# Kernel optimization log

Hardware: AMD Instinct MI355X
Metric: run time of the kernel (lower is better)

## Reference

```python
import jax, jax.numpy as jnp
import numpy as np

B, C, H, W = 4, 64, 64, 64
CQK = C // 8


def setup_inputs() -> dict:
    key = jax.random.key(0)
    ks = jax.random.split(key, 4)
    x = jax.random.normal(ks[0], (B, C, H, W), dtype=jnp.float32)
    Wq = jax.random.normal(ks[1], (CQK, C), dtype=jnp.float32) * (1.0 / np.sqrt(C))
    bq = jnp.zeros((CQK,), dtype=jnp.float32)
    Wk = jax.random.normal(ks[2], (CQK, C), dtype=jnp.float32) * (1.0 / np.sqrt(C))
    bk = jnp.zeros((CQK,), dtype=jnp.float32)
    Wv = jax.random.normal(ks[3], (C, C), dtype=jnp.float32) * (1.0 / np.sqrt(C))
    bv = jnp.zeros((C,), dtype=jnp.float32)
    gamma = jnp.ones((1,), dtype=jnp.float32)
    return {"x": x, "Wq": Wq, "bq": bq, "Wk": Wk, "bk": bk,
            "Wv": Wv, "bv": bv, "gamma": gamma}


def reference(x, Wq, bq, Wk, bk, Wv, bv, gamma):
    b, c, h, w = x.shape
    n = h * w
    xf = x.reshape(b, c, n)                      # [B, C, N]
    # 1x1 convs == per-pixel linear over channels
    q = jnp.einsum('oc,bcn->bon', Wq, xf) + bq[:, None]   # [B, C/8, N]
    k = jnp.einsum('oc,bcn->bon', Wk, xf) + bk[:, None]   # [B, C/8, N]
    v = jnp.einsum('oc,bcn->bon', Wv, xf) + bv[:, None]   # [B, C, N]
    # attention_map[b,i,j] = <q[:, i], k[:, j]>; softmax over j
    attn = jax.nn.softmax(jnp.einsum('bci,bcj->bij', q, k), axis=-1)  # [B, N, N]
    # out[b,c,i] = sum_j v[b,c,j] * attn[b,i,j]  (bmm(V, attn^T))
    out = jnp.einsum('bcj,bij->bci', v, attn).reshape(b, c, h, w)
    return gamma * out + x
```

## Files before the change

### kernel.cpp

```cpp
#include <hip/hip_runtime.h>
#include <hip/hip_bf16.h>
#include <math.h>

#define NPIX 4096

typedef __attribute__((ext_vector_type(8))) short s8;
typedef __attribute__((ext_vector_type(16))) float f16v;

static __device__ __forceinline__ unsigned packbf2(float a, float b) {
    union { __hip_bfloat162 h; unsigned u; } x;
    x.h = __float22bfloat162_rn(make_float2(a, b));
    return x.u;
}
static __device__ __forceinline__ float2 unpackbf2(unsigned u) {
    float lo = __uint_as_float(u << 16);
    float hi = __uint_as_float(u & 0xffff0000u);
    return make_float2(lo, hi);
}

__global__ __launch_bounds__(256) void prep_kernel(
    const float* __restrict__ x,
    const float* __restrict__ Wq, const float* __restrict__ bq,
    const float* __restrict__ Wk, const float* __restrict__ bk,
    __hip_bfloat16* __restrict__ qbf, __hip_bfloat16* __restrict__ kbf,
    __hip_bfloat16* __restrict__ xbf)
{
    __shared__ float Xp[64][65];
    int t = threadIdx.x;
    int lane = t & 63;
    int grp  = t >> 6;
    int b  = blockIdx.x >> 6;
    int n0 = (blockIdx.x & 63) << 6;

    const float* xb = x + ((size_t)b << 18);
    __hip_bfloat16* xbb = xbf + ((size_t)b << 18);
#pragma unroll
    for (int u = 0; u < 16; ++u) {
        int c = grp + u * 4;
        float v = xb[((size_t)c << 12) + n0 + lane];
        Xp[c][lane] = v;
        xbb[((size_t)c << 12) + n0 + lane] = __float2bfloat16(v);
    }
    __syncthreads();

    int o0 = grp * 2, o1 = o0 + 1;
    float qa0 = bq[o0], qa1 = bq[o1], ka0 = bk[o0], ka1 = bk[o1];
    const float* wq0 = Wq + o0 * 64; const float* wq1 = Wq + o1 * 64;
    const float* wk0 = Wk + o0 * 64; const float* wk1 = Wk + o1 * 64;
#pragma unroll
    for (int c = 0; c < 64; ++c) {
        float xv = Xp[c][lane];
        qa0 = fmaf(wq0[c], xv, qa0);
        qa1 = fmaf(wq1[c], xv, qa1);
        ka0 = fmaf(wk0[c], xv, ka0);
        ka1 = fmaf(wk1[c], xv, ka1);
    }
    qa0 *= 1.4426950408889634f;
    qa1 *= 1.4426950408889634f;
    int pix = b * NPIX + n0 + lane;
    *(__hip_bfloat162*)(qbf + (size_t)pix * 8 + o0) =
        __float22bfloat162_rn(make_float2(qa0, qa1));
    *(__hip_bfloat162*)(kbf + (size_t)pix * 8 + o0) =
        __float22bfloat162_rn(make_float2(ka0, ka1));
}

__global__ __launch_bounds__(256, 4) void flash_part_kernel(
    const __hip_bfloat16* __restrict__ qbf, const __hip_bfloat16* __restrict__ kbf,
    const __hip_bfloat16* __restrict__ xbf,
    __hip_bfloat16* __restrict__ Opart, float* __restrict__ Lp)
{
    __shared__ __align__(16) char pool[18432];
    unsigned short* PTs = (unsigned short*)pool;

    int t = threadIdx.x;
    int w    = t >> 6;
    int lane = t & 63;
    int l32  = lane & 31;
    int lh   = lane >> 5;
    int chalf = w & 1;
    int ihalf = w >> 1;

    int blk  = blockIdx.x;
    int sId  = blk >> 8;
    int rest = blk & 255;
    int b    = rest >> 6;
    int i0   = (rest & 63) << 6;
    int jbase = sId << 10;

    const s8 zero8 = {0, 0, 0, 0, 0, 0, 0, 0};

    s8 qf[2];
#pragma unroll
    for (int it32 = 0; it32 < 2; ++it32) {
        s8 qv = *(const s8*)(qbf + ((size_t)(b * NPIX + i0 + it32 * 32 + l32) << 3));
        qf[it32] = (lh == 0) ? qv : zero8;
    }

    f16v acc;
#pragma unroll
    for (int r = 0; r < 16; ++r) acc[r] = 0.f;
    f16v zero16;
#pragma unroll
    for (int r = 0; r < 16; ++r) zero16[r] = 0.f;
    float l[2] = {0.f, 0.f};

    const __hip_bfloat16* kb = kbf + ((size_t)(b * NPIX) << 3);
    const unsigned short* xg = (const unsigned short*)xbf + ((size_t)b << 18);
    const unsigned short* xrow = xg + ((size_t)(chalf * 32 + l32) << 12) + lh * 8;

    s8 kf = *(const s8*)(kb + ((size_t)(jbase + w * 32 + l32) << 3));

    for (int tile = 0; tile < 8; ++tile) {
        int j0 = jbase + (tile << 7);

        __syncthreads();

#pragma unroll
        for (int it32 = 0; it32 < 2; ++it32) {
            f16v sv = __builtin_amdgcn_mfma_f32_32x32x16_bf16(kf, qf[it32], zero16, 0, 0, 0);
            int i = it32 * 32 + l32;
            float ls = 0.f;
#pragma unroll
            for (int g = 0; g < 4; ++g) {
                float e0 = exp2f(sv[4 * g + 0]);
                float e1 = exp2f(sv[4 * g + 1]);
                float e2 = exp2f(sv[4 * g + 2]);
                float e3 = exp2f(sv[4 * g + 3]);
                ls += (e0 + e1) + (e2 + e3);
                uint2 pk;
                pk.x = packbf2(e0, e1); pk.y = packbf2(e2, e3);
                *(uint2*)(PTs + i * 136 + w * 32 + 8 * g + 4 * lh) = pk;
            }
            l[it32] += ls;
        }
        __syncthreads();

        {
            int jn = jbase + (((tile + 1) & 7) << 7);
            kf = *(const s8*)(kb + ((size_t)(jn + w * 32 + l32) << 3));
        }

#pragma unroll
        for (int q = 0; q < 8; ++q) {
            s8 xf = *(const s8*)(xrow + j0 + q * 16);
            s8 pf = *(const s8*)(PTs + (ihalf * 32 + l32) * 136 + q * 16 + lh * 8);
            acc = __builtin_amdgcn_mfma_f32_32x32x16_bf16(xf, pf, acc, 0, 0, 0);
        }
    }

    float* Osh = (float*)pool;
    float* Lsh = (float*)(pool + 17408);

#pragma unroll
    for (int it32 = 0; it32 < 2; ++it32)
        l[it32] += __shfl_xor(l[it32], 32);

    __syncthreads();
    if (lh == 0) {
#pragma unroll
        for (int it32 = 0; it32 < 2; ++it32)
            Lsh[w * 64 + it32 * 32 + l32] = l[it32];
    }
    {
        int i = ihalf * 32 + l32;
#pragma unroll
        for (int r = 0; r < 16; ++r) {
            int cc = chalf * 32 + (r & 3) + 8 * (r >> 2) + 4 * lh;
            Osh[i * 68 + cc] = acc[r];
        }
    }
    __syncthreads();

    if (t < 64)
        Lp[(size_t)blk * 64 + t] = Lsh[t] + Lsh[64 + t] + Lsh[128 + t] + Lsh[192 + t];

    {
        int i = t >> 2, c0 = (t & 3) << 4;
        const float* src = Osh + i * 68 + c0;
        uint4 lo, hi;
        lo.x = packbf2(src[0], src[1]);   lo.y = packbf2(src[2], src[3]);
        lo.z = packbf2(src[4], src[5]);   lo.w = packbf2(src[6], src[7]);
        hi.x = packbf2(src[8], src[9]);   hi.y = packbf2(src[10], src[11]);
        hi.z = packbf2(src[12], src[13]); hi.w = packbf2(src[14], src[15]);
        uint4* dst = (uint4*)(Opart + (size_t)blk * 4096 + i * 64 + c0);
        dst[0] = lo; dst[1] = hi;
    }
}

__global__ __launch_bounds__(256) void merge_kernel(
    const __hip_bfloat16* __restrict__ Opart, const float* __restrict__ Lp,
    const float* __restrict__ Wv, const float* __restrict__ bv,
    const float* __restrict__ x, const float* __restrict__ gamma,
    float* __restrict__ out)
{
    __shared__ float Osh[32 * 68];
    __shared__ float Wvs[4096];
    __shared__ float LinvS[32];
    __shared__ float bvs[64];

    int t = threadIdx.x;
    int m  = blockIdx.x;
    int b  = m >> 7;
    int i0 = (m & 127) << 5;

    if (t < 32) {
        int gi = i0 + t;
        int fb = b * 64 + (gi >> 6);
        int r  = gi & 63;
        float lt = Lp[(size_t)(0 * 256 + fb) * 64 + r]
                 + Lp[(size_t)(1 * 256 + fb) * 64 + r]
                 + Lp[(size_t)(2 * 256 + fb) * 64 + r]
                 + Lp[(size_t)(3 * 256 + fb) * 64 + r];
        LinvS[t] = 1.0f / lt;
    }
    if (t < 64) bvs[t] = bv[t];
    {
        const float4* wsrc = (const float4*)Wv;
        float4* wdst = (float4*)Wvs;
#pragma unroll
        for (int u = 0; u < 4; ++u) wdst[t + u * 256] = wsrc[t + u * 256];
    }
    __syncthreads();

    {
        int i = t >> 3, c0 = (t & 7) << 3;
        int gi = i0 + i;
        int fb = b * 64 + (gi >> 6);
        int r  = gi & 63;
        float o[8];
#pragma unroll
        for (int k = 0; k < 8; ++k) o[k] = 0.f;
#pragma unroll
        for (int sId = 0; sId < 4; ++sId) {
            size_t base = (size_t)(sId * 256 + fb) * 4096 + r * 64 + c0;
            uint4 pk = *(const uint4*)(Opart + base);
            float2 e0 = unpackbf2(pk.x), e1 = unpackbf2(pk.y);
            float2 e2 = unpackbf2(pk.z), e3 = unpackbf2(pk.w);
            o[0] += e0.x; o[1] += e0.y; o[2] += e1.x; o[3] += e1.y;
            o[4] += e2.x; o[5] += e2.y; o[6] += e3.x; o[7] += e3.y;
        }
        float* dst = Osh + i * 68 + c0;
        *(float4*)(dst + 0) = make_float4(o[0], o[1], o[2], o[3]);
        *(float4*)(dst + 4) = make_float4(o[4], o[5], o[6], o[7]);
    }
    __syncthreads();

    {
        int i  = t & 31;
        int cg = t >> 5;
        float inv = LinvS[i];
        float res[8];
#pragma unroll
        for (int k = 0; k < 8; ++k) res[k] = 0.f;
#pragma unroll 4
        for (int cb = 0; cb < 16; ++cb) {
            float4 o = *(const float4*)(Osh + i * 68 + cb * 4);
#pragma unroll
            for (int k = 0; k < 8; ++k) {
                float4 wv4 = *(const float4*)(Wvs + (cg * 8 + k) * 64 + cb * 4);
                res[k] = fmaf(wv4.x, o.x, fmaf(wv4.y, o.y, fmaf(wv4.z, o.z, fmaf(wv4.w, o.w, res[k]))));
            }
        }
        float g = gamma[0];
        const float* xr = x + ((size_t)b << 18) + i0;
        float* outp = out + ((size_t)b << 18) + i0;
#pragma unroll
        for (int k = 0; k < 8; ++k) {
            int cch = cg * 8 + k;
            float attn = fmaf(res[k], inv, bvs[cch]);
            size_t off = ((size_t)cch << 12) + i;
            outp[off] = fmaf(g, attn, xr[off]);
        }
    }
}

extern "C" void kernel_launch(void* const* d_in, const int* in_sizes, int n_in,
                              void* d_out, int out_size, void* d_ws, size_t ws_size,
                              hipStream_t stream) {
    const float* x     = (const float*)d_in[0];
    const float* Wq    = (const float*)d_in[1];
    const float* bq    = (const float*)d_in[2];
    const float* Wk    = (const float*)d_in[3];
    const float* bk    = (const float*)d_in[4];
    const float* Wv    = (const float*)d_in[5];
    const float* bv    = (const float*)d_in[6];
    const float* gamma = (const float*)d_in[7];
    float* out = (float*)d_out;

    __hip_bfloat16* qbf   = (__hip_bfloat16*)d_ws;
    __hip_bfloat16* kbf   = qbf + (size_t)4 * NPIX * 8;
    __hip_bfloat16* xbf   = kbf + (size_t)4 * NPIX * 8;
    __hip_bfloat16* Opart = xbf + (size_t)4 * NPIX * 64;
    float* Lp = (float*)(Opart + (size_t)1024 * 4096);

    prep_kernel<<<256, 256, 0, stream>>>(x, Wq, bq, Wk, bk, qbf, kbf, xbf);
    flash_part_kernel<<<1024, 256, 0, stream>>>(qbf, kbf, xbf, Opart, Lp);
    merge_kernel<<<512, 256, 0, stream>>>(Opart, Lp, Wv, bv, x, gamma, out);
}
```

Measured before the change: 117.8 us.

## Keep softmax probabilities in registers and stage X tiles through double-buffered LDS

```diff
diff --git a/kernel.cpp b/kernel.cpp
--- a/kernel.cpp
+++ b/kernel.cpp
@@ -5,6 +5,7 @@
 #define NPIX 4096
 
 typedef __attribute__((ext_vector_type(8))) short s8;
+typedef __attribute__((ext_vector_type(4))) short s4;
 typedef __attribute__((ext_vector_type(16))) float f16v;
 
 static __device__ __forceinline__ unsigned packbf2(float a, float b) {
@@ -64,21 +65,20 @@
         __float22bfloat162_rn(make_float2(ka0, ka1));
 }
 
-__global__ __launch_bounds__(256, 4) void flash_part_kernel(
+__global__ __launch_bounds__(512, 4) void flash_part_kernel(
     const __hip_bfloat16* __restrict__ qbf, const __hip_bfloat16* __restrict__ kbf,
     const __hip_bfloat16* __restrict__ xbf,
     __hip_bfloat16* __restrict__ Opart, float* __restrict__ Lp)
 {
-    __shared__ __align__(16) char pool[18432];
-    unsigned short* PTs = (unsigned short*)pool;
+    __shared__ __align__(16) char pool[35840];
 
     int t = threadIdx.x;
     int w    = t >> 6;
     int lane = t & 63;
     int l32  = lane & 31;
     int lh   = lane >> 5;
-    int chalf = w & 1;
-    int ihalf = w >> 1;
+    int g    = w >> 2;
+    int sw   = w & 3;
 
     int blk  = blockIdx.x;
     int sId  = blk >> 8;
@@ -89,101 +89,141 @@
 
     const s8 zero8 = {0, 0, 0, 0, 0, 0, 0, 0};
 
-    s8 qf[2];
-#pragma unroll
-    for (int it32 = 0; it32 < 2; ++it32) {
-        s8 qv = *(const s8*)(qbf + ((size_t)(b * NPIX + i0 + it32 * 32 + l32) << 3));
-        qf[it32] = (lh == 0) ? qv : zero8;
-    }
-
-    f16v acc;
-#pragma unroll
-    for (int r = 0; r < 16; ++r) acc[r] = 0.f;
+    s8 qf;
+    {
+        s8 qv = *(const s8*)(qbf + ((size_t)(b * NPIX + i0 + g * 32 + l32) << 3));
+        qf = (lh == 0) ? qv : zero8;
+    }
+
+    f16v acc[2];
     f16v zero16;
 #pragma unroll
-    for (int r = 0; r < 16; ++r) zero16[r] = 0.f;
-    float l[2] = {0.f, 0.f};
+    for (int r = 0; r < 16; ++r) { acc[0][r] = 0.f; acc[1][r] = 0.f; zero16[r] = 0.f; }
+    float lsum = 0.f;
 
     const __hip_bfloat16* kb = kbf + ((size_t)(b * NPIX) << 3);
     const unsigned short* xg = (const unsigned short*)xbf + ((size_t)b << 18);
-    const unsigned short* xrow = xg + ((size_t)(chalf * 32 + l32) << 12) + lh * 8;
-
-    s8 kf = *(const s8*)(kb + ((size_t)(jbase + w * 32 + l32) << 3));
-
+
+    int c = t >> 3, seg = t & 7;
+    const unsigned short* xsrc = xg + ((size_t)c << 12) + seg * 16;
+    int xdst = c * 140 + seg * 16;
+
+    uint2 sv0, sv1, sv2, sv3;
+    s8 kf;
+    {
+        const unsigned short* p = xsrc + jbase;
+        sv0 = *(const uint2*)(p);     sv1 = *(const uint2*)(p + 4);
+        sv2 = *(const uint2*)(p + 8); sv3 = *(const uint2*)(p + 12);
+        kf = *(const s8*)(kb + ((size_t)(jbase + sw * 32 + l32) << 3));
+    }
+
+    int bufp = 0;
     for (int tile = 0; tile < 8; ++tile) {
-        int j0 = jbase + (tile << 7);
-
-        __syncthreads();
-
-#pragma unroll
-        for (int it32 = 0; it32 < 2; ++it32) {
-            f16v sv = __builtin_amdgcn_mfma_f32_32x32x16_bf16(kf, qf[it32], zero16, 0, 0, 0);
-            int i = it32 * 32 + l32;
-            float ls = 0.f;
-#pragma unroll
-            for (int g = 0; g < 4; ++g) {
-                float e0 = exp2f(sv[4 * g + 0]);
-                float e1 = exp2f(sv[4 * g + 1]);
-                float e2 = exp2f(sv[4 * g + 2]);
-                float e3 = exp2f(sv[4 * g + 3]);
-                ls += (e0 + e1) + (e2 + e3);
-                uint2 pk;
-                pk.x = packbf2(e0, e1); pk.y = packbf2(e2, e3);
-                *(uint2*)(PTs + i * 136 + w * 32 + 8 * g + 4 * lh) = pk;
-            }
-            l[it32] += ls;
-        }
-        __syncthreads();
+        unsigned short* Xb = (unsigned short*)(pool + bufp * 17920);
+
+        *(uint2*)(Xb + xdst + 0)  = sv0;
+        *(uint2*)(Xb + xdst + 4)  = sv1;
+        *(uint2*)(Xb + xdst + 8)  = sv2;
+        *(uint2*)(Xb + xdst + 12) = sv3;
+
+        f16v sC = __builtin_amdgcn_mfma_f32_32x32x16_bf16(kf, qf, zero16, 0, 0, 0);
+        float e[16];
+#pragma unroll
+        for (int r = 0; r < 16; ++r) e[r] = exp2f(sC[r]);
+#pragma unroll
+        for (int r = 0; r < 16; ++r) lsum += e[r];
+        unsigned P2[8];
+#pragma unroll
+        for (int s = 0; s < 8; ++s) P2[s] = packbf2(e[2 * s], e[2 * s + 1]);
 
         {
             int jn = jbase + (((tile + 1) & 7) << 7);
-            kf = *(const s8*)(kb + ((size_t)(jn + w * 32 + l32) << 3));
-        }
-
-#pragma unroll
-        for (int q = 0; q < 8; ++q) {
-            s8 xf = *(const s8*)(xrow + j0 + q * 16);
-            s8 pf = *(const s8*)(PTs + (ihalf * 32 + l32) * 136 + q * 16 + lh * 8);
-            acc = __builtin_amdgcn_mfma_f32_32x32x16_bf16(xf, pf, acc, 0, 0, 0);
-        }
+            const unsigned short* p = xsrc + jn;
+            sv0 = *(const uint2*)(p);     sv1 = *(const uint2*)(p + 4);
+            sv2 = *(const uint2*)(p + 8); sv3 = *(const uint2*)(p + 12);
+            kf = *(const s8*)(kb + ((size_t)(jn + sw * 32 + l32) << 3));
+        }
+
+        __syncthreads();
+
+#if __has_builtin(__builtin_amdgcn_mfma_f32_32x32x8bf16_1k)
+#pragma unroll
+        for (int cm = 0; cm < 2; ++cm) {
+            const unsigned short* xrow = Xb + (cm * 32 + l32) * 140 + sw * 32 + lh * 4;
+#pragma unroll
+            for (int q = 0; q < 4; ++q) {
+                s4 xf = *(const s4*)(xrow + q * 8);
+                union { uint2 u; s4 v; } pu;
+                pu.u.x = P2[2 * q]; pu.u.y = P2[2 * q + 1];
+                acc[cm] = __builtin_amdgcn_mfma_f32_32x32x8bf16_1k(xf, pu.v, acc[cm], 0, 0, 0);
+            }
+        }
+#else
+        {
+            unsigned X0 = __shfl_xor(P2[0], 32), X1 = __shfl_xor(P2[1], 32);
+            unsigned X2 = __shfl_xor(P2[2], 32), X3 = __shfl_xor(P2[3], 32);
+            unsigned X4 = __shfl_xor(P2[4], 32), X5 = __shfl_xor(P2[5], 32);
+            unsigned X6 = __shfl_xor(P2[6], 32), X7 = __shfl_xor(P2[7], 32);
+            union { uint4 u[2]; s8 v[2]; } bf;
+            bf.u[0].x = lh ? X2 : P2[0]; bf.u[0].y = lh ? X3 : P2[1];
+            bf.u[0].z = lh ? P2[2] : X0; bf.u[0].w = lh ? P2[3] : X1;
+            bf.u[1].x = lh ? X6 : P2[4]; bf.u[1].y = lh ? X7 : P2[5];
+            bf.u[1].z = lh ? P2[6] : X4; bf.u[1].w = lh ? P2[7] : X5;
+#pragma unroll
+            for (int cm = 0; cm < 2; ++cm) {
+                const unsigned short* xrow = Xb + (cm * 32 + l32) * 140 + sw * 32 + lh * 8;
+#pragma unroll
+                for (int q = 0; q < 2; ++q) {
+                    union { uint2 u[2]; s8 v; } xu;
+                    xu.u[0] = *(const uint2*)(xrow + q * 16);
+                    xu.u[1] = *(const uint2*)(xrow + q * 16 + 4);
+                    acc[cm] = __builtin_amdgcn_mfma_f32_32x32x16_bf16(xu.v, bf.v[q], acc[cm], 0, 0, 0);
+                }
+            }
+        }
+#endif
+        bufp ^= 1;
     }
 
     float* Osh = (float*)pool;
-    float* Lsh = (float*)(pool + 17408);
-
-#pragma unroll
-    for (int it32 = 0; it32 < 2; ++it32)
-        l[it32] += __shfl_xor(l[it32], 32);
-
-    __syncthreads();
-    if (lh == 0) {
-#pragma unroll
-        for (int it32 = 0; it32 < 2; ++it32)
-            Lsh[w * 64 + it32 * 32 + l32] = l[it32];
-    }
-    {
-        int i = ihalf * 32 + l32;
-#pragma unroll
-        for (int r = 0; r < 16; ++r) {
-            int cc = chalf * 32 + (r & 3) + 8 * (r >> 2) + 4 * lh;
-            Osh[i * 68 + cc] = acc[r];
-        }
-    }
-    __syncthreads();
-
-    if (t < 64)
-        Lp[(size_t)blk * 64 + t] = Lsh[t] + Lsh[64 + t] + Lsh[128 + t] + Lsh[192 + t];
-
-    {
-        int i = t >> 2, c0 = (t & 3) << 4;
-        const float* src = Osh + i * 68 + c0;
-        uint4 lo, hi;
-        lo.x = packbf2(src[0], src[1]);   lo.y = packbf2(src[2], src[3]);
-        lo.z = packbf2(src[4], src[5]);   lo.w = packbf2(src[6], src[7]);
-        hi.x = packbf2(src[8], src[9]);   hi.y = packbf2(src[10], src[11]);
-        hi.z = packbf2(src[12], src[13]); hi.w = packbf2(src[14], src[15]);
-        uint4* dst = (uint4*)(Opart + (size_t)blk * 4096 + i * 64 + c0);
-        dst[0] = lo; dst[1] = hi;
+    float* Lsh = (float*)(pool + 35840 - 1024);
+
+    lsum += __shfl_xor(lsum, 32);
+
+    __syncthreads();
+    if (lh == 0) Lsh[w * 32 + l32] = lsum;
+
+    float* OshG = Osh + g * 2176;
+    for (int s = 0; s < 4; ++s) {
+        __syncthreads();
+        if (sw == s) {
+#pragma unroll
+            for (int cm = 0; cm < 2; ++cm)
+#pragma unroll
+                for (int r = 0; r < 16; ++r) {
+                    int cc = cm * 32 + (r & 3) + 8 * (r >> 2) + 4 * lh;
+                    float* p = OshG + l32 * 68 + cc;
+                    if (s == 0) *p = acc[cm][r];
+                    else        *p += acc[cm][r];
+                }
+        }
+    }
+    __syncthreads();
+
+    if (t < 64) {
+        int gi = t, gg = gi >> 5, ii = gi & 31;
+        Lp[(size_t)blk * 64 + gi] =
+            Lsh[(gg * 4 + 0) * 32 + ii] + Lsh[(gg * 4 + 1) * 32 + ii] +
+            Lsh[(gg * 4 + 2) * 32 + ii] + Lsh[(gg * 4 + 3) * 32 + ii];
+    }
+
+    {
+        int i = t >> 3, c0 = (t & 7) << 3;
+        const float* src = Osh + (i >> 5) * 2176 + (i & 31) * 68 + c0;
+        uint4 pk;
+        pk.x = packbf2(src[0], src[1]); pk.y = packbf2(src[2], src[3]);
+        pk.z = packbf2(src[4], src[5]); pk.w = packbf2(src[6], src[7]);
+        *(uint4*)(Opart + (size_t)blk * 4096 + i * 64 + c0) = pk;
     }
 }
 
@@ -294,6 +334,6 @@
     float* Lp = (float*)(Opart + (size_t)1024 * 4096);
 
     prep_kernel<<<256, 256, 0, stream>>>(x, Wq, bq, Wk, bk, qbf, kbf, xbf);
-    flash_part_kernel<<<1024, 256, 0, stream>>>(qbf, kbf, xbf, Opart, Lp);
+    flash_part_kernel<<<1024, 512, 0, stream>>>(qbf, kbf, xbf, Opart, Lp);
     merge_kernel<<<512, 256, 0, stream>>>(Opart, Lp, Wv, bv, x, gamma, out);
 }
```

Result: faster. 109.7 us (-6.9%).
